# Performance work log

Measured on AMD Instinct MI355X. Metric: run time of the kernel, lower is better.

## Reference

```python
import jax, jax.numpy as jnp
import numpy as np

SHIFT = 1  # (random.random() > 0.5) * 2 - 1 fixed to +1


def setup_inputs() -> dict:
    key = jax.random.key(0)
    k1, k2 = jax.random.split(key)
    x = jax.random.normal(k1, (1, 256, 14, 14), dtype=jnp.float32)
    w = jax.random.normal(k2, (256, 3, 3, 128), dtype=jnp.float32)  # learned param
    return {"x": x, "w": w}


def reference(x, w):
    s = SHIFT
    # 'ilkj -> ikjl': (1,256,14,14) -> (1,14,14,256)
    t = jnp.transpose(x, (0, 2, 3, 1))
    t = jnp.roll(t, s, axis=2)
    # unfold kernel (3,1), pad (1,0): treat axis1 as C=14, axis2 as H=14, axis3 as W=256.
    # Result layout (N, C, kh, H, W) matches torch's (1,14,3,14,256) reshape.
    tp = jnp.pad(t, ((0, 0), (0, 0), (1, 1), (0, 0)))
    t = jnp.stack([tp[:, :, a:a + 14, :] for a in range(3)], axis=2)  # (1,14,3,14,256)
    # split 256 -> (14,2,128) merged as 28, roll, split back, sum pair
    t = t.reshape(1, 14, 3, 28, 128)
    t = jnp.roll(t, s, axis=3)
    t = t.reshape(1, 14, 3, 14, 2, 128).sum(axis=4)  # (1,14,3,14,128)
    # second unfold (3,1), pad (1,0): here C=1, H=14 (axis1), W=3*14*128 flattened.
    tp = jnp.pad(t, ((0, 0), (1, 1), (0, 0), (0, 0), (0, 0)))
    t3 = jnp.stack([tp[:, a:a + 14] for a in range(3)], axis=1)  # (1,3,14,3,14,128)
    # contraction: m=1, j=3, n=14, k=3, o=14, l=128 ; w: (i=256, j=3, k=3, l=128)
    y = jnp.einsum('mjnkol,ijkl->mino', t3, w)  # (1,256,14,14)
    return y
```

## Files before the change

kernel.cpp:

```cpp
#include <hip/hip_runtime.h>
#include <hip/hip_bf16.h>


__device__ __forceinline__ float bf2f(unsigned short u) {
    union { unsigned int i; float f; } c; c.i = ((unsigned int)u) << 16; return c.f;
}
__device__ __forceinline__ unsigned short f2bf(float f) {
    __hip_bfloat16 b = __float2bfloat16(f);
    return *(unsigned short*)&b;
}

__global__ __launch_bounds__(256) void fused_shiftconv(
    const float* __restrict__ x,
    const float* __restrict__ w,
    float* __restrict__ out)
{
    __shared__ __align__(16) unsigned short rs[126 * 128];
    __shared__ __align__(16) float parts[112 * 66];

    const int n    = blockIdx.x;
    const int ig   = blockIdx.y;
    const int t    = threadIdx.x;
    const int lane = t & 63;
    const int wv   = t >> 6;

    const float* wbase = w + (ig * 8 + wv * 2) * 1152;
    float4 wq[2][4];
    float2 wt[2];
    #pragma unroll
    for (int ii = 0; ii < 2; ++ii) {
        const float* wp = wbase + ii * 1152;
        #pragma unroll
        for (int qi = 0; qi < 4; ++qi)
            wq[ii][qi] = *(const float4*)(wp + qi * 256 + lane * 4);
        wt[ii] = *(const float2*)(wp + 1024 + lane * 2);
    }

    #pragma unroll
    for (int item = 0; item < 2; ++item) {
        int j, l;
        if (item == 0) { j = t >> 7; l = t & 127; }
        else           { if (t >= 128) break; j = 2; l = t; }

        const int h = n + j - 1;
        float xlo[14], xhi[14];
        if ((unsigned)h < 14u) {
            const float* p0 = x + l * 196 + h * 14;
            const float* p1 = x + (128 + l) * 196 + h * 14;
            #pragma unroll
            for (int wi = 0; wi < 14; wi += 2) {
                float2 a = *(const float2*)(p0 + wi);
                float2 b = *(const float2*)(p1 + wi);
                xlo[wi] = a.x; xlo[wi + 1] = a.y;
                xhi[wi] = b.x; xhi[wi + 1] = b.y;
            }
        } else {
            #pragma unroll
            for (int wi = 0; wi < 14; ++wi) { xlo[wi] = 0.f; xhi[wi] = 0.f; }
        }
        #pragma unroll
        for (int k = 0; k < 3; ++k) {
            #pragma unroll
            for (int o = 0; o < 14; ++o) {
                float val = 0.f;
                const int wb = o + k - 1;
                if (wb >= 0 && wb < 14) val += xlo[wb ? wb - 1 : 13];
                const int v  = o ? o - 1 : 13;
                const int wa = v + k - 1;
                if (wa >= 0 && wa < 14) val += xhi[wa ? wa - 1 : 13];
                rs[((j * 3 + k) * 14 + o) * 128 + l] = f2bf(val);
            }
        }
    }
    __syncthreads();

    const int rbl   = (lane & 31) * 4;
    const int jkhi  = lane >> 5;
    const int prow0 = (wv * 2) * 14;
    #pragma unroll 2
    for (int o = 0; o < 14; ++o) {
        float rv[18];
        #pragma unroll
        for (int qi = 0; qi < 4; ++qi) {
            const int row = (qi * 2 + jkhi) * 14 + o;
            ushort4 u = *(const ushort4*)(rs + row * 128 + rbl);
            rv[qi * 4 + 0] = bf2f(u.x);
            rv[qi * 4 + 1] = bf2f(u.y);
            rv[qi * 4 + 2] = bf2f(u.z);
            rv[qi * 4 + 3] = bf2f(u.w);
        }
        {
            const int rowt = 112 + o;
            ushort2 ut = *(const ushort2*)(rs + rowt * 128 + lane * 2);
            rv[16] = bf2f(ut.x);
            rv[17] = bf2f(ut.y);
        }
        #pragma unroll
        for (int ii = 0; ii < 2; ++ii) {
            float a;
            a  = rv[0]  * wq[ii][0].x + rv[1]  * wq[ii][0].y + rv[2]  * wq[ii][0].z + rv[3]  * wq[ii][0].w;
            a += rv[4]  * wq[ii][1].x + rv[5]  * wq[ii][1].y + rv[6]  * wq[ii][1].z + rv[7]  * wq[ii][1].w;
            a += rv[8]  * wq[ii][2].x + rv[9]  * wq[ii][2].y + rv[10] * wq[ii][2].z + rv[11] * wq[ii][2].w;
            a += rv[12] * wq[ii][3].x + rv[13] * wq[ii][3].y + rv[14] * wq[ii][3].z + rv[15] * wq[ii][3].w;
            a += rv[16] * wt[ii].x + rv[17] * wt[ii].y;
            parts[(prow0 + ii * 14 + o) * 66 + lane] = a;
        }
    }
    __syncthreads();

    if (t < 112) {
        const float* pr = parts + t * 66;
        float s = 0.f;
        #pragma unroll
        for (int k2 = 0; k2 < 32; ++k2) {
            float2 v = *(const float2*)(pr + k2 * 2);
            s += v.x + v.y;
        }
        const int ii = t / 14;
        const int o  = t - ii * 14;
        const int i  = ig * 8 + ii;
        out[(i * 14 + n) * 14 + o] = s;
    }
}

extern "C" void kernel_launch(void* const* d_in, const int* in_sizes, int n_in,
                              void* d_out, int out_size, void* d_ws, size_t ws_size,
                              hipStream_t stream) {
    const float* x = (const float*)d_in[0];
    const float* w = (const float*)d_in[1];
    float* out = (float*)d_out;
    dim3 grid(14, 32);
    fused_shiftconv<<<grid, 256, 0, stream>>>(x, w, out);
}
```

Measured before the change: 62.82 us.

## Double output channels per block to halve redundant shift-buffer construction

Blocks now use 512 threads and cover 16 output channels instead of 8, so the grid shrinks from 14x32 to 14x16. Each bf16 shifted-input tile in shared memory is built half as often, and 384 threads build it in one pass instead of two. The partial-sum buffer gets stride 68 so the final reduction can use float4 loads. The cost is fewer blocks to spread across the GPU's compute units and more shared memory per block.

```diff
diff --git a/kernel.cpp b/kernel.cpp
--- a/kernel.cpp
+++ b/kernel.cpp
@@ -10,13 +10,15 @@
     return *(unsigned short*)&b;
 }
 
-__global__ __launch_bounds__(256) void fused_shiftconv(
+#define PSTRIDE 68
+
+__global__ __launch_bounds__(512) void fused_shiftconv(
     const float* __restrict__ x,
     const float* __restrict__ w,
     float* __restrict__ out)
 {
     __shared__ __align__(16) unsigned short rs[126 * 128];
-    __shared__ __align__(16) float parts[112 * 66];
+    __shared__ __align__(16) float parts[224 * PSTRIDE];
 
     const int n    = blockIdx.x;
     const int ig   = blockIdx.y;
@@ -24,7 +26,7 @@
     const int lane = t & 63;
     const int wv   = t >> 6;
 
-    const float* wbase = w + (ig * 8 + wv * 2) * 1152;
+    const float* wbase = w + (ig * 16 + wv * 2) * 1152;
     float4 wq[2][4];
     float2 wt[2];
     #pragma unroll
@@ -36,12 +38,9 @@
         wt[ii] = *(const float2*)(wp + 1024 + lane * 2);
     }
 
-    #pragma unroll
-    for (int item = 0; item < 2; ++item) {
-        int j, l;
-        if (item == 0) { j = t >> 7; l = t & 127; }
-        else           { if (t >= 128) break; j = 2; l = t; }
-
+    if (t < 384) {
+        const int j = t >> 7;
+        const int l = t & 127;
         const int h = n + j - 1;
         float xlo[14], xhi[14];
         if ((unsigned)h < 14u) {
@@ -76,7 +75,7 @@
 
     const int rbl   = (lane & 31) * 4;
     const int jkhi  = lane >> 5;
-    const int prow0 = (wv * 2) * 14;
+    const int prow0 = wv * 28;
     #pragma unroll 2
     for (int o = 0; o < 14; ++o) {
         float rv[18];
@@ -103,23 +102,27 @@
             a += rv[8]  * wq[ii][2].x + rv[9]  * wq[ii][2].y + rv[10] * wq[ii][2].z + rv[11] * wq[ii][2].w;
             a += rv[12] * wq[ii][3].x + rv[13] * wq[ii][3].y + rv[14] * wq[ii][3].z + rv[15] * wq[ii][3].w;
             a += rv[16] * wt[ii].x + rv[17] * wt[ii].y;
-            parts[(prow0 + ii * 14 + o) * 66 + lane] = a;
+            parts[(prow0 + ii * 14 + o) * PSTRIDE + lane] = a;
         }
     }
     __syncthreads();
 
-    if (t < 112) {
-        const float* pr = parts + t * 66;
-        float s = 0.f;
+    if (t < 224) {
+        const float* pr = parts + t * PSTRIDE;
+        float s0 = 0.f, s1 = 0.f;
         #pragma unroll
-        for (int k2 = 0; k2 < 32; ++k2) {
-            float2 v = *(const float2*)(pr + k2 * 2);
-            s += v.x + v.y;
+        for (int k2 = 0; k2 < 16; k2 += 2) {
+            float4 v0 = *(const float4*)(pr + k2 * 4);
+            float4 v1 = *(const float4*)(pr + k2 * 4 + 4);
+            s0 += v0.x + v0.y + v0.z + v0.w;
+            s1 += v1.x + v1.y + v1.z + v1.w;
         }
-        const int ii = t / 14;
-        const int o  = t - ii * 14;
-        const int i  = ig * 8 + ii;
-        out[(i * 14 + n) * 14 + o] = s;
+        const int wv2 = t / 28;
+        const int rem = t - wv2 * 28;
+        const int ii  = rem / 14;
+        const int o   = rem - ii * 14;
+        const int i   = ig * 16 + wv2 * 2 + ii;
+        out[(i * 14 + n) * 14 + o] = s0 + s1;
     }
 }
 
@@ -129,6 +132,6 @@
     const float* x = (const float*)d_in[0];
     const float* w = (const float*)d_in[1];
     float* out = (float*)d_out;
-    dim3 grid(14, 32);
-    fused_shiftconv<<<grid, 256, 0, stream>>>(x, w, out);
+    dim3 grid(14, 16);
+    fused_shiftconv<<<grid, 512, 0, stream>>>(x, w, out);
 }
```

Result: faster. 61.05 us (-2.8%).
